# Performance work log

Measured on AMD Instinct MI355X. Metric: run time of the kernel, lower is better.

## Reference

```python
import jax, jax.numpy as jnp
import numpy as np

MARGIN = 1.0


def setup_inputs() -> dict:
    key = jax.random.key(0)
    k1, k2 = jax.random.split(key)
    B, D, C = 8192, 128, 128
    embeddings = jax.random.normal(k1, (B, D), dtype=jnp.float32)
    labels = jax.random.randint(k2, (B,), 0, C, dtype=jnp.int64)
    return {"embeddings": embeddings, "labels": labels}


def _pairwise_dist(x):
    # Euclidean cdist with a sqrt-safe-at-zero formulation (diag is exactly 0).
    sq = jnp.sum(x * x, axis=-1)
    d2 = jnp.maximum(sq[:, None] + sq[None, :] - 2.0 * (x @ x.T), 0.0)
    pos = d2 > 0
    return jnp.where(pos, jnp.sqrt(jnp.where(pos, d2, 1.0)), 0.0)


def reference(embeddings, labels):
    B = embeddings.shape[0]
    dist = _pairwise_dist(embeddings)  # [B, B]
    same = labels[:, None] == labels[None, :]  # [B, B]
    eye = jnp.eye(B, dtype=bool)
    is_pos = same & ~eye
    is_neg = ~same
    neg_inf = jnp.float32(-jnp.inf)
    pos_inf = jnp.float32(jnp.inf)
    hardest_pos = jnp.max(jnp.where(is_pos, dist, neg_inf), axis=1)  # [B]
    hardest_neg = jnp.min(jnp.where(is_neg, dist, pos_inf), axis=1)  # [B]
    valid = jnp.any(is_pos, axis=1) & jnp.any(is_neg, axis=1)
    per_row = jax.nn.relu(hardest_pos - hardest_neg + MARGIN)
    n_valid = jnp.sum(valid)
    loss = jnp.sum(jnp.where(valid, per_row, 0.0)) / jnp.maximum(n_valid, 1).astype(embeddings.dtype)
    # matches torch fallback of 0.0 when no valid anchors exist
    return jnp.where(n_valid > 0, loss, jnp.float32(0.0))
```

## Files before the change

### kernel.cpp

```cpp
#include <hip/hip_runtime.h>
#include <hip/hip_bf16.h>

typedef __attribute__((ext_vector_type(8))) short short8;
typedef __attribute__((ext_vector_type(4))) float floatx4;
typedef __attribute__((ext_vector_type(2))) float floatx2;

#define B_ROWS 8192
#define DIM    128
#define NSPLIT 16
#define JSPAN  (B_ROWS / NSPLIT)
#define NTILE  (JSPAN / 16)
#define WAVES  4
#define RPW    64
#define BM     (WAVES * RPW)
#define NRB    (B_ROWS / BM)
#define BIAS   4096.0f


#define OFF_SQ    (2u << 20)
#define OFF_SQLAB (OFF_SQ + (64u << 10))
#define OFF_D2P   (OFF_SQLAB + (64u << 10))
#define OFF_D2N   (OFF_D2P + (512u << 10))
#define OFF_ACC   (OFF_D2N + (512u << 10))

#define GLOAD_LDS(g, l) __builtin_amdgcn_global_load_lds(                     \
    (const __attribute__((address_space(1))) void*)(g),                       \
    (__attribute__((address_space(3))) void*)(l), 16, 0, 0)

__global__ __launch_bounds__(256) void prep_kernel(const float* __restrict__ x,
                                                   const int* __restrict__ lab,
                                                   __hip_bfloat16* __restrict__ xf,
                                                   float* __restrict__ sq,
                                                   float2* __restrict__ sqlab,
                                                   float* __restrict__ acc_sum,
                                                   int* __restrict__ done) {
    if (blockIdx.x == 0 && threadIdx.x == 0) { acc_sum[0] = 0.f; done[0] = 0; }
    const int row  = blockIdx.x * 4 + (threadIdx.x >> 6);
    const int lane = threadIdx.x & 63;
    const float2 v = *reinterpret_cast<const float2*>(x + row * DIM + lane * 2);
    __hip_bfloat162 b2;
    b2.x = __float2bfloat16(v.x);
    b2.y = __float2bfloat16(v.y);
    const int kk = lane >> 4;
    const int g  = (lane >> 2) & 3;
    const int e  = (lane & 3) * 2;
    const int idx = (row >> 4) * 2048 + kk * 512 + (g * 16 + (row & 15)) * 8 + e;
    *reinterpret_cast<__hip_bfloat162*>(xf + idx) = b2;
    float s = v.x * v.x + v.y * v.y;
    #pragma unroll
    for (int m = 1; m < 64; m <<= 1) s += __shfl_xor(s, m, 64);
    if (lane == 0) {
        sq[row] = s;
        float2 p; p.x = s; p.y = __int_as_float(lab[row]);
        sqlab[row] = p;
    }
}

__global__ __launch_bounds__(256, 2) void main_kernel(
    const __hip_bfloat16* __restrict__ xf,
    const float* __restrict__ sq,
    const int*  __restrict__ lab,
    const float2* __restrict__ sqlab,
    float* __restrict__ d2p,
    float* __restrict__ d2n) {
    __shared__ __align__(16) char ldsT[4][4096];
    __shared__ __align__(16) char ldsS[4096];

    const int tid  = threadIdx.x;
    const int lane = tid & 63;
    const int wave = tid >> 6;
    const int l15  = lane & 15;
    const int g    = lane >> 4;
    const int rowbase = blockIdx.x * BM + wave * RPW;
    const int split   = blockIdx.y;
    const int jstart  = split * JSPAN;

    {
        const char* gs = (const char*)sqlab + (size_t)jstart * 8;
        GLOAD_LDS(gs + tid * 16, &ldsS[wave * 1024]);
        const char* gt = (const char*)xf + (size_t)(jstart >> 4) * 4096;
        GLOAD_LDS(gt +      tid * 16, &ldsT[0][wave * 1024]);
        GLOAD_LDS(gt + 4096 + tid * 16, &ldsT[1][wave * 1024]);
        GLOAD_LDS(gt + 8192 + tid * 16, &ldsT[2][wave * 1024]);
    }

    short8 a[4][4];
    #pragma unroll
    for (int s = 0; s < 4; ++s) {
        const __hip_bfloat16* ap = xf + ((size_t)(rowbase >> 4) + s) * 2048 + lane * 8;
        #pragma unroll
        for (int kk = 0; kk < 4; ++kk)
            a[s][kk] = *reinterpret_cast<const short8*>(ap + kk * 512);
    }
    int labi[4][4];
    #pragma unroll
    for (int s = 0; s < 4; ++s)
        #pragma unroll
        for (int q = 0; q < 4; ++q)
            labi[s][q] = lab[rowbase + s * 16 + g * 4 + q];

    float mx[4][4], mn[4][4];
    #pragma unroll
    for (int s = 0; s < 4; ++s)
        #pragma unroll
        for (int q = 0; q < 4; ++q) { mx[s][q] = -INFINITY; mn[s][q] = INFINITY; }

    #define STAGE(buf_, tile_) GLOAD_LDS(                                     \
        (const char*)xf + ((size_t)(jstart >> 4) + (unsigned)(tile_)) * 4096  \
            + tid * 16,                                                       \
        &ldsT[buf_][wave * 1024])

    for (int jt = 0; jt < NTILE; ++jt) {
        asm volatile("s_waitcnt vmcnt(2)" ::: "memory");
        __builtin_amdgcn_s_barrier();
        STAGE((jt + 3) & 3, (jt + 3) & 31);

        const int buf = jt & 3;
        short8 b[4];
        #pragma unroll
        for (int kk = 0; kk < 4; ++kk)
            b[kk] = *reinterpret_cast<const short8*>(&ldsT[buf][kk * 1024 + lane * 16]);
        const floatx2 sl = *reinterpret_cast<const floatx2*>(&ldsS[(jt * 16 + l15) * 8]);
        const float sqj  = sl[0];
        const int   labj = __float_as_int(sl[1]);

        floatx4 acc[4];
        #pragma unroll
        for (int s = 0; s < 4; ++s) acc[s] = (floatx4){0.f, 0.f, 0.f, 0.f};
        #pragma unroll
        for (int kk = 0; kk < 4; ++kk) {
            #pragma unroll
            for (int s = 0; s < 4; ++s)
                acc[s] = __builtin_amdgcn_mfma_f32_16x16x32_bf16(a[s][kk], b[kk], acc[s], 0, 0, 0);
        }

        const float sqjb = sqj + BIAS;
        #pragma unroll
        for (int s = 0; s < 4; ++s) {
            #pragma unroll
            for (int q = 0; q < 4; ++q) {
                const float t = fmaf(-2.f, acc[s][q], (labj == labi[s][q]) ? sqjb : sqj);
                mx[s][q] = fmaxf(mx[s][q], t);
                mn[s][q] = fminf(mn[s][q], t);
            }
        }
    }
    #undef STAGE

    #pragma unroll
    for (int s = 0; s < 4; ++s)
        #pragma unroll
        for (int q = 0; q < 4; ++q) {
            #pragma unroll
            for (int mk = 1; mk < 16; mk <<= 1) {
                mx[s][q] = fmaxf(mx[s][q], __shfl_xor(mx[s][q], mk, 64));
                mn[s][q] = fminf(mn[s][q], __shfl_xor(mn[s][q], mk, 64));
            }
        }
    if (l15 == 0) {
        #pragma unroll
        for (int s = 0; s < 4; ++s)
            #pragma unroll
            for (int q = 0; q < 4; ++q) {
                const int i = rowbase + s * 16 + g * 4 + q;
                const float sqi = sq[i];
                d2p[split * B_ROWS + i] = sqi + (mx[s][q] - BIAS);
                d2n[split * B_ROWS + i] = sqi + mn[s][q];
            }
    }
}

__global__ __launch_bounds__(256) void combine_kernel(
    const float* __restrict__ d2p, const float* __restrict__ d2n,
    float* __restrict__ acc_sum, int* __restrict__ done,
    float* __restrict__ out) {
    const int row = blockIdx.x * 256 + threadIdx.x;
    float p = -INFINITY, n = INFINITY;
    #pragma unroll
    for (int s = 0; s < NSPLIT; ++s) {
        p = fmaxf(p, d2p[s * B_ROWS + row]);
        n = fminf(n, d2n[s * B_ROWS + row]);
    }
    float v = fmaxf(sqrtf(fmaxf(p, 0.f)) - sqrtf(fmaxf(n, 0.f)) + 1.0f, 0.f);
    #pragma unroll
    for (int mk = 1; mk < 64; mk <<= 1) v += __shfl_xor(v, mk, 64);
    __shared__ float sv[4];
    const int wv = threadIdx.x >> 6;
    if ((threadIdx.x & 63) == 0) sv[wv] = v;
    __syncthreads();
    if (threadIdx.x == 0) {
        atomicAdd(acc_sum, sv[0] + sv[1] + sv[2] + sv[3]);
        __threadfence();
        const int old = atomicAdd(done, 1);
        if (old == (int)gridDim.x - 1) {
            const float fs = atomicAdd(acc_sum, 0.f);
            out[0] = fs / (float)B_ROWS;
        }
    }
}

extern "C" void kernel_launch(void* const* d_in, const int* in_sizes, int n_in,
                              void* d_out, int out_size, void* d_ws, size_t ws_size,
                              hipStream_t stream) {
    const float* x   = (const float*)d_in[0];
    const int*   lab = (const int*)d_in[1];
    float*       out = (float*)d_out;

    char* ws = (char*)d_ws;
    __hip_bfloat16* xf = (__hip_bfloat16*)ws;
    float*  sq      = (float*)(ws + OFF_SQ);
    float2* sqlab   = (float2*)(ws + OFF_SQLAB);
    float*  d2p     = (float*)(ws + OFF_D2P);
    float*  d2n     = (float*)(ws + OFF_D2N);
    float*  acc_sum = (float*)(ws + OFF_ACC);
    int*    done    = (int*)(ws + OFF_ACC + 4);

    prep_kernel<<<B_ROWS / 4, 256, 0, stream>>>(x, lab, xf, sq, sqlab, acc_sum, done);
    main_kernel<<<dim3(NRB, NSPLIT), 256, 0, stream>>>(xf, sq, lab, sqlab, d2p, d2n);
    combine_kernel<<<B_ROWS / 256, 256, 0, stream>>>(d2p, d2n, acc_sum, done, out);
}
```

Before: 43.08 us.

## Give each wave a private triple-buffered LDS ring to drop per-tile block barriers

The block-shared four-slot LDS tile buffer is replaced with a separate three-slot ring for each wave. Each wave now loads the whole 4KB column tile itself and waits only on its own vmcnt, so the block-wide s_barrier in every tile iteration is gone. A single __syncthreads after the prologue covers the shared sq/label strip, which wave 0 now loads alone. In exchange, each block reads every B tile from global/L2 four times instead of once, and LDS use grows to about 52KB per block. That could limit residency or make the kernel bandwidth-bound on L2.

```diff
diff --git a/kernel.cpp b/kernel.cpp
--- a/kernel.cpp
+++ b/kernel.cpp
@@ -63,7 +63,7 @@
     const float2* __restrict__ sqlab,
     float* __restrict__ d2p,
     float* __restrict__ d2n) {
-    __shared__ __align__(16) char ldsT[4][4096];
+    __shared__ __align__(16) char ring[WAVES][3][4096];
     __shared__ __align__(16) char ldsS[4096];
 
     const int tid  = threadIdx.x;
@@ -75,13 +75,20 @@
     const int split   = blockIdx.y;
     const int jstart  = split * JSPAN;
 
-    {
+    const char* tilebase = (const char*)xf + (size_t)(jstart >> 4) * 4096;
+
+    #pragma unroll
+    for (int t = 0; t < 3; ++t) {
+        #pragma unroll
+        for (int p = 0; p < 4; ++p)
+            GLOAD_LDS(tilebase + (size_t)t * 4096 + p * 1024 + lane * 16,
+                      &ring[wave][t][p * 1024]);
+    }
+    if (wave == 0) {
         const char* gs = (const char*)sqlab + (size_t)jstart * 8;
-        GLOAD_LDS(gs + tid * 16, &ldsS[wave * 1024]);
-        const char* gt = (const char*)xf + (size_t)(jstart >> 4) * 4096;
-        GLOAD_LDS(gt +      tid * 16, &ldsT[0][wave * 1024]);
-        GLOAD_LDS(gt + 4096 + tid * 16, &ldsT[1][wave * 1024]);
-        GLOAD_LDS(gt + 8192 + tid * 16, &ldsT[2][wave * 1024]);
+        #pragma unroll
+        for (int p = 0; p < 4; ++p)
+            GLOAD_LDS(gs + p * 1024 + lane * 16, &ldsS[p * 1024]);
     }
 
     short8 a[4][4];
@@ -105,21 +112,23 @@
         #pragma unroll
         for (int q = 0; q < 4; ++q) { mx[s][q] = -INFINITY; mn[s][q] = INFINITY; }
 
-    #define STAGE(buf_, tile_) GLOAD_LDS(                                     \
-        (const char*)xf + ((size_t)(jstart >> 4) + (unsigned)(tile_)) * 4096  \
-            + tid * 16,                                                       \
-        &ldsT[buf_][wave * 1024])
+    __syncthreads();
 
     for (int jt = 0; jt < NTILE; ++jt) {
-        asm volatile("s_waitcnt vmcnt(2)" ::: "memory");
-        __builtin_amdgcn_s_barrier();
-        STAGE((jt + 3) & 3, (jt + 3) & 31);
-
-        const int buf = jt & 3;
+        const int snext = (jt + 2) % 3;
+        const unsigned tnext = (unsigned)((jt + 2) & 31);
+        #pragma unroll
+        for (int p = 0; p < 4; ++p)
+            GLOAD_LDS(tilebase + (size_t)tnext * 4096 + p * 1024 + lane * 16,
+                      &ring[wave][snext][p * 1024]);
+
+        asm volatile("s_waitcnt vmcnt(8)" ::: "memory");
+
+        const int slot = jt % 3;
         short8 b[4];
         #pragma unroll
         for (int kk = 0; kk < 4; ++kk)
-            b[kk] = *reinterpret_cast<const short8*>(&ldsT[buf][kk * 1024 + lane * 16]);
+            b[kk] = *reinterpret_cast<const short8*>(&ring[wave][slot][kk * 1024 + lane * 16]);
         const floatx2 sl = *reinterpret_cast<const floatx2*>(&ldsS[(jt * 16 + l15) * 8]);
         const float sqj  = sl[0];
         const int   labj = __float_as_int(sl[1]);
@@ -145,7 +154,6 @@
             }
         }
     }
-    #undef STAGE
 
     #pragma unroll
     for (int s = 0; s < 4; ++s)
```

Result: slower. 44.79 us (+4.0%).
